# Optimization experiments

Hardware: AMD Instinct MI355X
Metric: run time of the kernel (lower is better)

Reference implementation:

```python
import jax, jax.numpy as jnp
import numpy as np

B, NH, NQ, NK, D = 2, 12, 2048, 2048, 64


def setup_inputs() -> dict:
    k0 = jax.random.key(0)
    k1, k2, k3, k4 = jax.random.split(k0, 4)
    return {
        "query": jax.random.normal(k1, (B, NH, NQ, D), dtype=jnp.float32),
        "key": jax.random.normal(k2, (B, NH, NK, D), dtype=jnp.float32),
        "value": jax.random.normal(k3, (B, NH, NK, D), dtype=jnp.float32),
        "mask": jnp.zeros((B, 1, NQ, NK), dtype=jnp.float32),
        "bias": jax.random.normal(k4, (NQ + NK + 1, NH), dtype=jnp.float32) * 0.02,
    }


def reference(query, key, value, mask, bias):
    head_size = query.shape[-1]
    nq = query.shape[-2]
    nk = key.shape[-2]
    # scores [B, H, Q, K]
    qk = jnp.einsum("bhqd,bhkd->bhqk", query, key) / jnp.sqrt(jnp.float32(head_size)).astype(query.dtype)
    # relative position bias: table [(nq+nk+1), nh] gathered at pos_q - pos_k + nk
    pos_qk = jnp.arange(nq)[:, None] - jnp.arange(nk)[None, :] + nk  # [Q, K]
    bias_qk = bias[pos_qk]                      # [Q, K, H]
    bias_qk = jnp.transpose(bias_qk, (2, 0, 1))[None]  # [1, H, Q, K]
    qk = qk + bias_qk + mask
    attn = jax.nn.softmax(qk, axis=-1)
    return jnp.einsum("bhqk,bhkd->bhqd", attn, value)
```

## Files before the change

### kernel.cpp

```cpp
#include <hip/hip_runtime.h>

#define NB  2
#define NH  12
#define NQ  2048
#define NKV 2048
#define DH  64
#define KVB 64
#define BH  (NB * NH)

#define L2E 1.44269504088896f
#define QSCL (0.125f * L2E)

typedef __attribute__((ext_vector_type(8))) short bf16x8;
typedef __attribute__((ext_vector_type(4))) short bf16x4;
typedef __attribute__((ext_vector_type(4))) float f32x4;
typedef __attribute__((ext_vector_type(2))) unsigned short u16x2;

#define EXP2F(x) __builtin_amdgcn_exp2f(x)

#define WS_KB   0u
#define WS_VT   6291456u
#define WS_NEED 12582912u

__device__ __forceinline__ unsigned short f2bf(float f) {
    unsigned int u = __float_as_uint(f);
    u += 0x7FFFu + ((u >> 16) & 1u);
    return (unsigned short)(u >> 16);
}
__device__ __forceinline__ float bf2f(unsigned short h) {
    return __uint_as_float((unsigned int)h << 16);
}
__device__ __forceinline__ int permk6(int k6) {
    return (k6 & 32) + ((k6 & 12) << 1) + ((k6 & 16) >> 2) + (k6 & 3);
}

__global__ __launch_bounds__(256)
void conv_kv(const float* __restrict__ K, const float* __restrict__ V,
             unsigned short* __restrict__ Kb, unsigned short* __restrict__ Vt)
{
    const int tid = threadIdx.x;
    const int kvt = blockIdx.x & 31;
    const int bh  = blockIdx.x >> 5;
    const int kv0 = kvt * 64;

    const float* ksrc = K + ((size_t)bh * NKV + kv0) * DH;
    const float* vsrc = V + ((size_t)bh * NKV + kv0) * DH;
    unsigned short* kdst = Kb + ((size_t)bh * NKV + kv0) * DH;
    unsigned short* vdst = Vt + (size_t)bh * DH * NKV + kv0;

    __shared__ float Ts[64][65];

#pragma unroll
    for (int p = 0; p < 2; ++p) {
        const int ch = p * 256 + tid;
        const int row = ch >> 3, c8 = (ch & 7) * 8;
        const float4 f0 = *(const float4*)(ksrc + (size_t)row * DH + c8);
        const float4 f1 = *(const float4*)(ksrc + (size_t)row * DH + c8 + 4);
        bf16x8 o;
        o[0] = (short)f2bf(f0.x); o[1] = (short)f2bf(f0.y);
        o[2] = (short)f2bf(f0.z); o[3] = (short)f2bf(f0.w);
        o[4] = (short)f2bf(f1.x); o[5] = (short)f2bf(f1.y);
        o[6] = (short)f2bf(f1.z); o[7] = (short)f2bf(f1.w);
        *(bf16x8*)(kdst + (size_t)row * DH + c8) = o;
    }
#pragma unroll
    for (int p = 0; p < 4; ++p) {
        const int fi = p * 1024 + tid * 4;
        const int row = fi >> 6, col = fi & 63;
        const float4 f = *(const float4*)(vsrc + (size_t)row * DH + col);
        Ts[row][col] = f.x; Ts[row][col + 1] = f.y;
        Ts[row][col + 2] = f.z; Ts[row][col + 3] = f.w;
    }
    __syncthreads();
#pragma unroll
    for (int p = 0; p < 2; ++p) {
        const int ch = p * 256 + tid;
        const int d = ch >> 3, c8 = (ch & 7) * 8;
        bf16x8 o;
#pragma unroll
        for (int j = 0; j < 8; ++j) o[j] = (short)f2bf(Ts[c8 + j][d]);
        unsigned short* vrow = vdst + (size_t)d * NKV;
        *(uint2*)(vrow + permk6(c8))     = ((const uint2*)&o)[0];
        *(uint2*)(vrow + permk6(c8 + 4)) = ((const uint2*)&o)[1];
    }
}

#define ARENA_BYTES 45312
#define KS_OFF 8448
#define VS_OFF 26880
#define BUF_STRIDE 9216

__global__ __launch_bounds__(512, 2)
void attn_fwd(const unsigned short* __restrict__ Kb, const unsigned short* __restrict__ Vt,
              const float* __restrict__ Q, const float* __restrict__ M,
              const float* __restrict__ Bias, float* __restrict__ O)
{
    const int tid  = threadIdx.x;
    const int w    = tid >> 6;
    const int wq   = w >> 1;
    const int wk   = w & 1;
    const int lane = tid & 63;
    const int l16  = lane & 15;
    const int g    = lane >> 4;

    const int qt = blockIdx.x & 31;
    const int bh = blockIdx.x >> 5;
    const int h  = bh % NH;
    const int b  = bh / NH;
    const int q0 = qt * 64;

    __shared__ __align__(16) char arena[ARENA_BYTES];
    unsigned short* bias2 = (unsigned short*)arena;

    for (int x = tid; x < 2112; x += 512) {
        const unsigned short v = f2bf(L2E * Bias[(size_t)(q0 + 1 + x) * NH + h]);
        bias2[2111 - x] = v;
        if (x <= 2110) bias2[2112 + 2110 - x] = v;
    }

    const float* qptr = Q + ((size_t)bh * NQ + q0 + wq * 16 + l16) * DH;
    bf16x8 qa[2];
#pragma unroll
    for (int dc = 0; dc < 2; ++dc) {
        const float4 f0 = *(const float4*)(qptr + dc * 32 + g * 8);
        const float4 f1 = *(const float4*)(qptr + dc * 32 + g * 8 + 4);
        qa[dc][0] = (short)f2bf(f0.x * QSCL); qa[dc][1] = (short)f2bf(f0.y * QSCL);
        qa[dc][2] = (short)f2bf(f0.z * QSCL); qa[dc][3] = (short)f2bf(f0.w * QSCL);
        qa[dc][4] = (short)f2bf(f1.x * QSCL); qa[dc][5] = (short)f2bf(f1.y * QSCL);
        qa[dc][6] = (short)f2bf(f1.z * QSCL); qa[dc][7] = (short)f2bf(f1.w * QSCL);
    }

    f32x4 o[4];
#pragma unroll
    for (int nt = 0; nt < 4; ++nt) { o[nt][0]=0.f; o[nt][1]=0.f; o[nt][2]=0.f; o[nt][3]=0.f; }
    float m_r = -1e30f;
    float l_r = 0.f;

    const unsigned short* kbB = Kb + (size_t)bh * NKV * DH;
    const unsigned short* vtB = Vt + (size_t)bh * DH * NKV;
    const float* mbase = M + (size_t)b * NQ * NKV
                           + (size_t)(q0 + wq * 16 + l16) * NKV + wk * 32 + g * 4;

    const int srow = tid >> 3, sc8 = (tid & 7) * 8;
    const int ldoff = srow * 144 + sc8 * 2;

    bf16x8 krB, vrB;
    float4 mr4[2], mrn4[2];
    krB = *(const bf16x8*)(kbB + (size_t)srow * DH + sc8);
    vrB = *(const bf16x8*)(vtB + (size_t)srow * NKV + sc8);
#pragma unroll
    for (int nt = 0; nt < 2; ++nt) mr4[nt] = *(const float4*)(mbase + nt * 16);

    *(bf16x8*)(arena + KS_OFF + ldoff) = krB;
    *(bf16x8*)(arena + VS_OFF + ldoff) = vrB;
    krB = *(const bf16x8*)(kbB + (size_t)(64 + srow) * DH + sc8);
    vrB = *(const bf16x8*)(vtB + (size_t)srow * NKV + 64 + sc8);
    __syncthreads();

    int cur = 0;
    for (int t = 0; t < NKV / KVB; ++t) {
        const int kv0 = t * KVB;
        const int tn  = ((t + 1) & (NKV / KVB - 1)) * KVB;
        const int t2  = ((t + 2) & (NKV / KVB - 1)) * KVB;
        const int nxt = cur ^ 1;

        *(bf16x8*)(arena + KS_OFF + nxt * BUF_STRIDE + ldoff) = krB;
        *(bf16x8*)(arena + VS_OFF + nxt * BUF_STRIDE + ldoff) = vrB;
        krB = *(const bf16x8*)(kbB + (size_t)(t2 + srow) * DH + sc8);
        vrB = *(const bf16x8*)(vtB + (size_t)srow * NKV + t2 + sc8);
#pragma unroll
        for (int nt = 0; nt < 2; ++nt) mrn4[nt] = *(const float4*)(mbase + tn + nt * 16);

        const unsigned short (*Ks)[72] = (const unsigned short(*)[72])(arena + KS_OFF + cur * BUF_STRIDE);
        const unsigned short (*Vs)[72] = (const unsigned short(*)[72])(arena + VS_OFF + cur * BUF_STRIDE);

        f32x4 s[2];
#pragma unroll
        for (int nt = 0; nt < 2; ++nt) {
            f32x4 acc; acc[0]=0.f; acc[1]=0.f; acc[2]=0.f; acc[3]=0.f;
            const int kvrow = wk * 32 + nt * 16 + l16;
            const bf16x8 kb0 = *(const bf16x8*)(&Ks[kvrow][g * 8]);
            const bf16x8 kb1 = *(const bf16x8*)(&Ks[kvrow][32 + g * 8]);
            acc = __builtin_amdgcn_mfma_f32_16x16x32_bf16(kb0, qa[0], acc, 0, 0, 0);
            acc = __builtin_amdgcn_mfma_f32_16x16x32_bf16(kb1, qa[1], acc, 0, 0, 0);
            s[nt] = acc;
        }

        bf16x8 va2[4];
#pragma unroll
        for (int nt = 0; nt < 4; ++nt)
            va2[nt] = *(const bf16x8*)(&Vs[nt * 16 + l16][wk * 32 + g * 8]);

        const int ib0 = (wq * 16 + l16) - (kv0 + wk * 32 + g * 4) + 2047;
#pragma unroll
        for (int nt = 0; nt < 2; ++nt) {
            const int j0 = 2111 - (ib0 - nt * 16);
            const int r  = j0 & 1;
            const unsigned short* bp = bias2 + r * 2112 + (j0 - r);
            const u16x2 b01 = *(const u16x2*)(bp);
            const u16x2 b23 = *(const u16x2*)(bp + 2);
            s[nt][0] += __fmaf_rn(nt ? mr4[1].x : mr4[0].x, L2E, bf2f(b01[0]));
            s[nt][1] += __fmaf_rn(nt ? mr4[1].y : mr4[0].y, L2E, bf2f(b01[1]));
            s[nt][2] += __fmaf_rn(nt ? mr4[1].z : mr4[0].z, L2E, bf2f(b23[0]));
            s[nt][3] += __fmaf_rn(nt ? mr4[1].w : mr4[0].w, L2E, bf2f(b23[1]));
        }

        const float x0  = fmaxf(fmaxf(s[0][0], s[0][1]), s[0][2]);
        const float x1  = fmaxf(fmaxf(s[0][3], s[1][0]), s[1][1]);
        const float x2  = fmaxf(s[1][2], s[1][3]);
        const float lmx = fmaxf(fmaxf(x0, x1), x2);
        if (__any(lmx > m_r + 8.0f)) {
            float mx = lmx;
            mx = fmaxf(mx, __shfl_xor(mx, 16));
            mx = fmaxf(mx, __shfl_xor(mx, 32));
            const float mn = fmaxf(m_r, mx);
            const float alpha = EXP2F(m_r - mn);
            m_r = mn;
            l_r *= alpha;
#pragma unroll
            for (int nt = 0; nt < 4; ++nt) {
                o[nt][0] *= alpha; o[nt][1] *= alpha;
                o[nt][2] *= alpha; o[nt][3] *= alpha;
            }
        }
        f32x4 pv[2];
#pragma unroll
        for (int nt = 0; nt < 2; ++nt) {
            pv[nt][0] = EXP2F(s[nt][0] - m_r);
            pv[nt][1] = EXP2F(s[nt][1] - m_r);
            pv[nt][2] = EXP2F(s[nt][2] - m_r);
            pv[nt][3] = EXP2F(s[nt][3] - m_r);
        }
        l_r += ((pv[0][0] + pv[0][1]) + (pv[0][2] + pv[0][3]))
             + ((pv[1][0] + pv[1][1]) + (pv[1][2] + pv[1][3]));

        mr4[0] = mrn4[0]; mr4[1] = mrn4[1];

        union { unsigned u[4]; bf16x8 v; } pb8;
        asm("v_cvt_pk_bf16_f32 %0, %1, %2" : "=v"(pb8.u[0]) : "v"(pv[0][0]), "v"(pv[0][1]));
        asm("v_cvt_pk_bf16_f32 %0, %1, %2" : "=v"(pb8.u[1]) : "v"(pv[0][2]), "v"(pv[0][3]));
        asm("v_cvt_pk_bf16_f32 %0, %1, %2" : "=v"(pb8.u[2]) : "v"(pv[1][0]), "v"(pv[1][1]));
        asm("v_cvt_pk_bf16_f32 %0, %1, %2" : "=v"(pb8.u[3]) : "v"(pv[1][2]), "v"(pv[1][3]));

#pragma unroll
        for (int nt = 0; nt < 4; ++nt)
            o[nt] = __builtin_amdgcn_mfma_f32_16x16x32_bf16(va2[nt], pb8.v, o[nt], 0, 0, 0);

        __syncthreads();
        cur = nxt;
    }

    l_r += __shfl_xor(l_r, 16);
    l_r += __shfl_xor(l_r, 32);

    float (*mO)[64][17] = (float(*)[64][17])(arena + KS_OFF);
    float* mML          = (float*)(arena + KS_OFF + 17408);

    __syncthreads();
    if (wk == 1) {
#pragma unroll
        for (int nt = 0; nt < 4; ++nt) {
#pragma unroll
            for (int reg = 0; reg < 4; ++reg)
                mO[wq][nt * 16 + g * 4 + reg][l16] = o[nt][reg];
        }
        if (g == 0) {
            mML[wq * 16 + l16]      = m_r;
            mML[64 + wq * 16 + l16] = l_r;
        }
    }
    __syncthreads();
    if (wk == 0) {
        const float m1 = mML[wq * 16 + l16];
        const float l1 = mML[64 + wq * 16 + l16];
        const float mn = fmaxf(m_r, m1);
        const float a0 = EXP2F(m_r - mn);
        const float a1 = EXP2F(m1 - mn);
        const float inv = 1.f / (l_r * a0 + l1 * a1);
        float* obase = O + ((size_t)bh * NQ + q0 + wq * 16 + l16) * DH;
#pragma unroll
        for (int nt = 0; nt < 4; ++nt) {
            float4 ov;
            ov.x = (o[nt][0] * a0 + mO[wq][nt * 16 + g * 4 + 0][l16] * a1) * inv;
            ov.y = (o[nt][1] * a0 + mO[wq][nt * 16 + g * 4 + 1][l16] * a1) * inv;
            ov.z = (o[nt][2] * a0 + mO[wq][nt * 16 + g * 4 + 2][l16] * a1) * inv;
            ov.w = (o[nt][3] * a0 + mO[wq][nt * 16 + g * 4 + 3][l16] * a1) * inv;
            *(float4*)(obase + nt * 16 + g * 4) = ov;
        }
    }
}

__global__ __launch_bounds__(256, 3)
void attn_full(const float* __restrict__ Q, const float* __restrict__ K,
               const float* __restrict__ V, const float* __restrict__ M,
               const float* __restrict__ Bias, float* __restrict__ O)
{
    const int tid  = threadIdx.x;
    const int wv   = tid >> 6;
    const int lane = tid & 63;
    const int l16  = lane & 15;
    const int g    = lane >> 4;

    const int qt = blockIdx.x & 31;
    const int h  = (blockIdx.x >> 5) % NH;
    const int b  = blockIdx.x / (32 * NH);
    const int q0 = qt * 64;

    __shared__ float bias_s[2112];
    __shared__ unsigned short Ks[64][72];
    __shared__ unsigned short Vs[64][72];
    __shared__ unsigned short Ps[4][16][72];

    for (int i = tid; i < 2112; i += 256)
        bias_s[i] = Bias[(size_t)(q0 + 1 + i) * NH + h];

    const float* qptr = Q + (((size_t)b * NH + h) * NQ + q0 + wv * 16 + l16) * DH;
    bf16x8 qa[2];
#pragma unroll
    for (int dc = 0; dc < 2; ++dc) {
        const float4 f0 = *(const float4*)(qptr + dc * 32 + g * 8);
        const float4 f1 = *(const float4*)(qptr + dc * 32 + g * 8 + 4);
        qa[dc][0] = (short)f2bf(f0.x); qa[dc][1] = (short)f2bf(f0.y);
        qa[dc][2] = (short)f2bf(f0.z); qa[dc][3] = (short)f2bf(f0.w);
        qa[dc][4] = (short)f2bf(f1.x); qa[dc][5] = (short)f2bf(f1.y);
        qa[dc][6] = (short)f2bf(f1.z); qa[dc][7] = (short)f2bf(f1.w);
    }

    f32x4 o[4];
#pragma unroll
    for (int nt = 0; nt < 4; ++nt) { o[nt][0]=0.f; o[nt][1]=0.f; o[nt][2]=0.f; o[nt][3]=0.f; }
    float m_r[4] = {-1e30f, -1e30f, -1e30f, -1e30f};
    float l_r[4] = {0.f, 0.f, 0.f, 0.f};

    const float* kbase = K + ((size_t)b * NH + h) * NKV * DH;
    const float* vbase = V + ((size_t)b * NH + h) * NKV * DH;
    const float* mrow[4];
#pragma unroll
    for (int r = 0; r < 4; ++r)
        mrow[r] = M + (size_t)b * NQ * NKV + (size_t)(q0 + wv * 16 + g * 4 + r) * NKV + l16;

    const int r0 = tid >> 4, c0 = (tid & 15) * 4;

    float4 kr[4], vr[4];
    float  mr[4][4];
#pragma unroll
    for (int i = 0; i < 4; ++i) {
        kr[i] = *(const float4*)(kbase + (size_t)(i * 16 + r0) * DH + c0);
        vr[i] = *(const float4*)(vbase + (size_t)(i * 16 + r0) * DH + c0);
    }
#pragma unroll
    for (int r = 0; r < 4; ++r)
#pragma unroll
        for (int nt = 0; nt < 4; ++nt) mr[r][nt] = mrow[r][nt * 16];

    for (int t = 0; t < NKV / 64; ++t) {
        const int kv0 = t * 64;
        const int kvn = ((t + 1) & 31) * 64;

        __syncthreads();
#pragma unroll
        for (int i = 0; i < 4; ++i) {
            unsigned short* dst = &Ks[i * 16 + r0][c0];
            dst[0] = f2bf(kr[i].x); dst[1] = f2bf(kr[i].y);
            dst[2] = f2bf(kr[i].z); dst[3] = f2bf(kr[i].w);
        }
#pragma unroll
        for (int i = 0; i < 4; ++i) {
            const int rr = i * 16 + r0;
            Vs[c0 + 0][rr] = f2bf(vr[i].x); Vs[c0 + 1][rr] = f2bf(vr[i].y);
            Vs[c0 + 2][rr] = f2bf(vr[i].z); Vs[c0 + 3][rr] = f2bf(vr[i].w);
        }
#pragma unroll
        for (int i = 0; i < 4; ++i) {
            kr[i] = *(const float4*)(kbase + (size_t)(kvn + i * 16 + r0) * DH + c0);
            vr[i] = *(const float4*)(vbase + (size_t)(kvn + i * 16 + r0) * DH + c0);
        }
        __syncthreads();

        f32x4 s[4];
#pragma unroll
        for (int nt = 0; nt < 4; ++nt) {
            f32x4 acc; acc[0]=0.f; acc[1]=0.f; acc[2]=0.f; acc[3]=0.f;
            const bf16x8 kb0 = *(const bf16x8*)(&Ks[nt * 16 + l16][g * 8]);
            const bf16x8 kb1 = *(const bf16x8*)(&Ks[nt * 16 + l16][32 + g * 8]);
            acc = __builtin_amdgcn_mfma_f32_16x16x32_bf16(qa[0], kb0, acc, 0, 0, 0);
            acc = __builtin_amdgcn_mfma_f32_16x16x32_bf16(qa[1], kb1, acc, 0, 0, 0);
            s[nt] = acc;
        }

#pragma unroll
        for (int r = 0; r < 4; ++r) {
            const int qr = wv * 16 + g * 4 + r;
#pragma unroll
            for (int nt = 0; nt < 4; ++nt) {
                float x = s[nt][r] * 0.125f + mr[r][nt];
                x += bias_s[qr - (kv0 + nt * 16 + l16) + 2047];
                s[nt][r] = x;
            }
            float mx = fmaxf(fmaxf(s[0][r], s[1][r]), fmaxf(s[2][r], s[3][r]));
            mx = fmaxf(mx, __shfl_xor(mx, 1));
            mx = fmaxf(mx, __shfl_xor(mx, 2));
            mx = fmaxf(mx, __shfl_xor(mx, 4));
            mx = fmaxf(mx, __shfl_xor(mx, 8));
            const float mo = m_r[r];
            const float mn = fmaxf(mo, mx);
            m_r[r] = mn;
            const float alpha = __expf(mo - mn);
            float p[4], rs = 0.f;
#pragma unroll
            for (int nt = 0; nt < 4; ++nt) { p[nt] = __expf(s[nt][r] - mn); rs += p[nt]; }
            rs += __shfl_xor(rs, 1);
            rs += __shfl_xor(rs, 2);
            rs += __shfl_xor(rs, 4);
            rs += __shfl_xor(rs, 8);
            l_r[r] = l_r[r] * alpha + rs;
#pragma unroll
            for (int nt = 0; nt < 4; ++nt) o[nt][r] *= alpha;
#pragma unroll
            for (int nt = 0; nt < 4; ++nt)
                Ps[wv][g * 4 + r][nt * 16 + l16] = f2bf(p[nt]);
        }

#pragma unroll
        for (int r = 0; r < 4; ++r)
#pragma unroll
            for (int nt = 0; nt < 4; ++nt) mr[r][nt] = mrow[r][kvn + nt * 16];

#pragma unroll
        for (int kc = 0; kc < 2; ++kc) {
            const bf16x8 pa = *(const bf16x8*)(&Ps[wv][l16][kc * 32 + g * 8]);
#pragma unroll
            for (int nt = 0; nt < 4; ++nt) {
                const bf16x8 vb = *(const bf16x8*)(&Vs[nt * 16 + l16][kc * 32 + g * 8]);
                o[nt] = __builtin_amdgcn_mfma_f32_16x16x32_bf16(pa, vb, o[nt], 0, 0, 0);
            }
        }
    }

    float* obase = O + (((size_t)b * NH + h) * NQ + q0 + wv * 16) * DH;
#pragma unroll
    for (int r = 0; r < 4; ++r) {
        const float inv = 1.f / l_r[r];
#pragma unroll
        for (int nt = 0; nt < 4; ++nt)
            obase[(size_t)(g * 4 + r) * DH + nt * 16 + l16] = o[nt][r] * inv;
    }
}

extern "C" void kernel_launch(void* const* d_in, const int* in_sizes, int n_in,
                              void* d_out, int out_size, void* d_ws, size_t ws_size,
                              hipStream_t stream) {
    const float* Q    = (const float*)d_in[0];
    const float* K    = (const float*)d_in[1];
    const float* V    = (const float*)d_in[2];
    const float* M    = (const float*)d_in[3];
    const float* Bias = (const float*)d_in[4];
    float* O = (float*)d_out;

    if (ws_size >= (size_t)WS_NEED) {
        unsigned short* Kb = (unsigned short*)((char*)d_ws + WS_KB);
        unsigned short* Vt = (unsigned short*)((char*)d_ws + WS_VT);
        conv_kv<<<dim3(BH * 32), dim3(256), 0, stream>>>(K, V, Kb, Vt);
        attn_fwd<<<dim3(BH * 32), dim3(512), 0, stream>>>(Kb, Vt, Q, M, Bias, O);
    } else {
        attn_full<<<dim3(BH * 32), dim3(256), 0, stream>>>(Q, K, V, M, Bias, O);
    }
}
```

Measured before the change: 78.31 us.

## Halve block to 256 threads with each wave handling two query sub-tiles

Each workgroup shrinks from 8 to 4 waves, and every wave now processes two 16-row query sub-tiles against the same K/V fragments it reads from LDS. This reuses each LDS read of K and V across two MFMA chains and halves the per-block LDS read traffic per query row. In exchange, register pressure per wave goes up (two sets of accumulators, scores and masks), each thread stages two rows of K/V per tile, and there are fewer waves per block to hide latency.

```diff
diff --git a/kernel.cpp b/kernel.cpp
--- a/kernel.cpp
+++ b/kernel.cpp
@@ -90,14 +90,14 @@
 #define VS_OFF 26880
 #define BUF_STRIDE 9216
 
-__global__ __launch_bounds__(512, 2)
+__global__ __launch_bounds__(256, 2)
 void attn_fwd(const unsigned short* __restrict__ Kb, const unsigned short* __restrict__ Vt,
               const float* __restrict__ Q, const float* __restrict__ M,
               const float* __restrict__ Bias, float* __restrict__ O)
 {
     const int tid  = threadIdx.x;
     const int w    = tid >> 6;
-    const int wq   = w >> 1;
+    const int qp   = w >> 1;
     const int wk   = w & 1;
     const int lane = tid & 63;
     const int l16  = lane & 15;
@@ -112,49 +112,64 @@
     __shared__ __align__(16) char arena[ARENA_BYTES];
     unsigned short* bias2 = (unsigned short*)arena;
 
-    for (int x = tid; x < 2112; x += 512) {
+    for (int x = tid; x < 2112; x += 256) {
         const unsigned short v = f2bf(L2E * Bias[(size_t)(q0 + 1 + x) * NH + h]);
         bias2[2111 - x] = v;
         if (x <= 2110) bias2[2112 + 2110 - x] = v;
     }
 
-    const float* qptr = Q + ((size_t)bh * NQ + q0 + wq * 16 + l16) * DH;
-    bf16x8 qa[2];
-#pragma unroll
-    for (int dc = 0; dc < 2; ++dc) {
-        const float4 f0 = *(const float4*)(qptr + dc * 32 + g * 8);
-        const float4 f1 = *(const float4*)(qptr + dc * 32 + g * 8 + 4);
-        qa[dc][0] = (short)f2bf(f0.x * QSCL); qa[dc][1] = (short)f2bf(f0.y * QSCL);
-        qa[dc][2] = (short)f2bf(f0.z * QSCL); qa[dc][3] = (short)f2bf(f0.w * QSCL);
-        qa[dc][4] = (short)f2bf(f1.x * QSCL); qa[dc][5] = (short)f2bf(f1.y * QSCL);
-        qa[dc][6] = (short)f2bf(f1.z * QSCL); qa[dc][7] = (short)f2bf(f1.w * QSCL);
-    }
-
-    f32x4 o[4];
-#pragma unroll
-    for (int nt = 0; nt < 4; ++nt) { o[nt][0]=0.f; o[nt][1]=0.f; o[nt][2]=0.f; o[nt][3]=0.f; }
-    float m_r = -1e30f;
-    float l_r = 0.f;
+    bf16x8 qa[2][2];
+#pragma unroll
+    for (int sub = 0; sub < 2; ++sub) {
+        const float* qptr = Q + ((size_t)bh * NQ + q0 + qp * 32 + sub * 16 + l16) * DH;
+#pragma unroll
+        for (int dc = 0; dc < 2; ++dc) {
+            const float4 f0 = *(const float4*)(qptr + dc * 32 + g * 8);
+            const float4 f1 = *(const float4*)(qptr + dc * 32 + g * 8 + 4);
+            qa[sub][dc][0] = (short)f2bf(f0.x * QSCL); qa[sub][dc][1] = (short)f2bf(f0.y * QSCL);
+            qa[sub][dc][2] = (short)f2bf(f0.z * QSCL); qa[sub][dc][3] = (short)f2bf(f0.w * QSCL);
+            qa[sub][dc][4] = (short)f2bf(f1.x * QSCL); qa[sub][dc][5] = (short)f2bf(f1.y * QSCL);
+            qa[sub][dc][6] = (short)f2bf(f1.z * QSCL); qa[sub][dc][7] = (short)f2bf(f1.w * QSCL);
+        }
+    }
+
+    f32x4 o0[4], o1[4];
+#pragma unroll
+    for (int nt = 0; nt < 4; ++nt) {
+        o0[nt][0]=0.f; o0[nt][1]=0.f; o0[nt][2]=0.f; o0[nt][3]=0.f;
+        o1[nt][0]=0.f; o1[nt][1]=0.f; o1[nt][2]=0.f; o1[nt][3]=0.f;
+    }
+    float m_r[2] = {-1e30f, -1e30f};
+    float l_r[2] = {0.f, 0.f};
 
     const unsigned short* kbB = Kb + (size_t)bh * NKV * DH;
     const unsigned short* vtB = Vt + (size_t)bh * DH * NKV;
-    const float* mbase = M + (size_t)b * NQ * NKV
-                           + (size_t)(q0 + wq * 16 + l16) * NKV + wk * 32 + g * 4;
+    const float* mb0 = M + (size_t)b * NQ * NKV
+                         + (size_t)(q0 + qp * 32 + l16) * NKV + wk * 32 + g * 4;
+    const float* mb1 = mb0 + 16 * NKV;
 
     const int srow = tid >> 3, sc8 = (tid & 7) * 8;
-    const int ldoff = srow * 144 + sc8 * 2;
-
-    bf16x8 krB, vrB;
-    float4 mr4[2], mrn4[2];
-    krB = *(const bf16x8*)(kbB + (size_t)srow * DH + sc8);
-    vrB = *(const bf16x8*)(vtB + (size_t)srow * NKV + sc8);
-#pragma unroll
-    for (int nt = 0; nt < 2; ++nt) mr4[nt] = *(const float4*)(mbase + nt * 16);
-
-    *(bf16x8*)(arena + KS_OFF + ldoff) = krB;
-    *(bf16x8*)(arena + VS_OFF + ldoff) = vrB;
-    krB = *(const bf16x8*)(kbB + (size_t)(64 + srow) * DH + sc8);
-    vrB = *(const bf16x8*)(vtB + (size_t)srow * NKV + 64 + sc8);
+
+    bf16x8 krB[2], vrB[2];
+    float4 mr4[2][2], mrn4[2][2];
+#pragma unroll
+    for (int p = 0; p < 2; ++p) {
+        krB[p] = *(const bf16x8*)(kbB + (size_t)(p * 32 + srow) * DH + sc8);
+        vrB[p] = *(const bf16x8*)(vtB + (size_t)(p * 32 + srow) * NKV + sc8);
+    }
+#pragma unroll
+    for (int nt = 0; nt < 2; ++nt) {
+        mr4[0][nt] = *(const float4*)(mb0 + nt * 16);
+        mr4[1][nt] = *(const float4*)(mb1 + nt * 16);
+    }
+#pragma unroll
+    for (int p = 0; p < 2; ++p) {
+        const int ldoff = (p * 32 + srow) * 144 + sc8 * 2;
+        *(bf16x8*)(arena + KS_OFF + ldoff) = krB[p];
+        *(bf16x8*)(arena + VS_OFF + ldoff) = vrB[p];
+        krB[p] = *(const bf16x8*)(kbB + (size_t)(64 + p * 32 + srow) * DH + sc8);
+        vrB[p] = *(const bf16x8*)(vtB + (size_t)(p * 32 + srow) * NKV + 64 + sc8);
+    }
     __syncthreads();
 
     int cur = 0;
@@ -164,94 +179,132 @@
         const int t2  = ((t + 2) & (NKV / KVB - 1)) * KVB;
         const int nxt = cur ^ 1;
 
-        *(bf16x8*)(arena + KS_OFF + nxt * BUF_STRIDE + ldoff) = krB;
-        *(bf16x8*)(arena + VS_OFF + nxt * BUF_STRIDE + ldoff) = vrB;
-        krB = *(const bf16x8*)(kbB + (size_t)(t2 + srow) * DH + sc8);
-        vrB = *(const bf16x8*)(vtB + (size_t)srow * NKV + t2 + sc8);
-#pragma unroll
-        for (int nt = 0; nt < 2; ++nt) mrn4[nt] = *(const float4*)(mbase + tn + nt * 16);
+#pragma unroll
+        for (int p = 0; p < 2; ++p) {
+            const int ldoff = (p * 32 + srow) * 144 + sc8 * 2;
+            *(bf16x8*)(arena + KS_OFF + nxt * BUF_STRIDE + ldoff) = krB[p];
+            *(bf16x8*)(arena + VS_OFF + nxt * BUF_STRIDE + ldoff) = vrB[p];
+            krB[p] = *(const bf16x8*)(kbB + (size_t)(t2 + p * 32 + srow) * DH + sc8);
+            vrB[p] = *(const bf16x8*)(vtB + (size_t)(p * 32 + srow) * NKV + t2 + sc8);
+        }
+#pragma unroll
+        for (int nt = 0; nt < 2; ++nt) {
+            mrn4[0][nt] = *(const float4*)(mb0 + tn + nt * 16);
+            mrn4[1][nt] = *(const float4*)(mb1 + tn + nt * 16);
+        }
 
         const unsigned short (*Ks)[72] = (const unsigned short(*)[72])(arena + KS_OFF + cur * BUF_STRIDE);
         const unsigned short (*Vs)[72] = (const unsigned short(*)[72])(arena + VS_OFF + cur * BUF_STRIDE);
 
-        f32x4 s[2];
+        bf16x8 kb0[2], kb1[2];
 #pragma unroll
         for (int nt = 0; nt < 2; ++nt) {
-            f32x4 acc; acc[0]=0.f; acc[1]=0.f; acc[2]=0.f; acc[3]=0.f;
             const int kvrow = wk * 32 + nt * 16 + l16;
-            const bf16x8 kb0 = *(const bf16x8*)(&Ks[kvrow][g * 8]);
-            const bf16x8 kb1 = *(const bf16x8*)(&Ks[kvrow][32 + g * 8]);
-            acc = __builtin_amdgcn_mfma_f32_16x16x32_bf16(kb0, qa[0], acc, 0, 0, 0);
-            acc = __builtin_amdgcn_mfma_f32_16x16x32_bf16(kb1, qa[1], acc, 0, 0, 0);
-            s[nt] = acc;
-        }
-
+            kb0[nt] = *(const bf16x8*)(&Ks[kvrow][g * 8]);
+            kb1[nt] = *(const bf16x8*)(&Ks[kvrow][32 + g * 8]);
+        }
         bf16x8 va2[4];
 #pragma unroll
         for (int nt = 0; nt < 4; ++nt)
             va2[nt] = *(const bf16x8*)(&Vs[nt * 16 + l16][wk * 32 + g * 8]);
 
-        const int ib0 = (wq * 16 + l16) - (kv0 + wk * 32 + g * 4) + 2047;
+        f32x4 s0[2], s1[2];
 #pragma unroll
         for (int nt = 0; nt < 2; ++nt) {
-            const int j0 = 2111 - (ib0 - nt * 16);
-            const int r  = j0 & 1;
-            const unsigned short* bp = bias2 + r * 2112 + (j0 - r);
-            const u16x2 b01 = *(const u16x2*)(bp);
-            const u16x2 b23 = *(const u16x2*)(bp + 2);
-            s[nt][0] += __fmaf_rn(nt ? mr4[1].x : mr4[0].x, L2E, bf2f(b01[0]));
-            s[nt][1] += __fmaf_rn(nt ? mr4[1].y : mr4[0].y, L2E, bf2f(b01[1]));
-            s[nt][2] += __fmaf_rn(nt ? mr4[1].z : mr4[0].z, L2E, bf2f(b23[0]));
-            s[nt][3] += __fmaf_rn(nt ? mr4[1].w : mr4[0].w, L2E, bf2f(b23[1]));
-        }
-
-        const float x0  = fmaxf(fmaxf(s[0][0], s[0][1]), s[0][2]);
-        const float x1  = fmaxf(fmaxf(s[0][3], s[1][0]), s[1][1]);
-        const float x2  = fmaxf(s[1][2], s[1][3]);
-        const float lmx = fmaxf(fmaxf(x0, x1), x2);
-        if (__any(lmx > m_r + 8.0f)) {
-            float mx = lmx;
-            mx = fmaxf(mx, __shfl_xor(mx, 16));
-            mx = fmaxf(mx, __shfl_xor(mx, 32));
-            const float mn = fmaxf(m_r, mx);
-            const float alpha = EXP2F(m_r - mn);
-            m_r = mn;
-            l_r *= alpha;
-#pragma unroll
-            for (int nt = 0; nt < 4; ++nt) {
-                o[nt][0] *= alpha; o[nt][1] *= alpha;
-                o[nt][2] *= alpha; o[nt][3] *= alpha;
-            }
-        }
-        f32x4 pv[2];
+            f32x4 a0; a0[0]=0.f; a0[1]=0.f; a0[2]=0.f; a0[3]=0.f;
+            f32x4 a1 = a0;
+            a0 = __builtin_amdgcn_mfma_f32_16x16x32_bf16(kb0[nt], qa[0][0], a0, 0, 0, 0);
+            a0 = __builtin_amdgcn_mfma_f32_16x16x32_bf16(kb1[nt], qa[0][1], a0, 0, 0, 0);
+            a1 = __builtin_amdgcn_mfma_f32_16x16x32_bf16(kb0[nt], qa[1][0], a1, 0, 0, 0);
+            a1 = __builtin_amdgcn_mfma_f32_16x16x32_bf16(kb1[nt], qa[1][1], a1, 0, 0, 0);
+            s0[nt] = a0; s1[nt] = a1;
+        }
+
+        const int qbase = qp * 32 + l16 - (kv0 + wk * 32 + g * 4) + 2047;
+#pragma unroll
+        for (int sub = 0; sub < 2; ++sub) {
+            f32x4* s = sub ? s1 : s0;
+#pragma unroll
+            for (int nt = 0; nt < 2; ++nt) {
+                const int j0 = 2111 - (qbase + sub * 16 - nt * 16);
+                const int r  = j0 & 1;
+                const unsigned short* bp = bias2 + r * 2112 + (j0 - r);
+                const u16x2 b01 = *(const u16x2*)(bp);
+                const u16x2 b23 = *(const u16x2*)(bp + 2);
+                const float4 mm = mr4[sub][nt];
+                s[nt][0] += __fmaf_rn(mm.x, L2E, bf2f(b01[0]));
+                s[nt][1] += __fmaf_rn(mm.y, L2E, bf2f(b01[1]));
+                s[nt][2] += __fmaf_rn(mm.z, L2E, bf2f(b23[0]));
+                s[nt][3] += __fmaf_rn(mm.w, L2E, bf2f(b23[1]));
+            }
+        }
+
+        f32x4 pv0[2], pv1[2];
+#pragma unroll
+        for (int sub = 0; sub < 2; ++sub) {
+            f32x4* s  = sub ? s1 : s0;
+            f32x4* pv = sub ? pv1 : pv0;
+            f32x4* oo = sub ? o1 : o0;
+            const float x0  = fmaxf(fmaxf(s[0][0], s[0][1]), s[0][2]);
+            const float x1  = fmaxf(fmaxf(s[0][3], s[1][0]), s[1][1]);
+            const float x2  = fmaxf(s[1][2], s[1][3]);
+            const float lmx = fmaxf(fmaxf(x0, x1), x2);
+            if (__any(lmx > m_r[sub] + 8.0f)) {
+                float mx = lmx;
+                mx = fmaxf(mx, __shfl_xor(mx, 16));
+                mx = fmaxf(mx, __shfl_xor(mx, 32));
+                const float mn = fmaxf(m_r[sub], mx);
+                const float alpha = EXP2F(m_r[sub] - mn);
+                m_r[sub] = mn;
+                l_r[sub] *= alpha;
+#pragma unroll
+                for (int nt = 0; nt < 4; ++nt) {
+                    oo[nt][0] *= alpha; oo[nt][1] *= alpha;
+                    oo[nt][2] *= alpha; oo[nt][3] *= alpha;
+                }
+            }
+#pragma unroll
+            for (int nt = 0; nt < 2; ++nt) {
+                pv[nt][0] = EXP2F(s[nt][0] - m_r[sub]);
+                pv[nt][1] = EXP2F(s[nt][1] - m_r[sub]);
+                pv[nt][2] = EXP2F(s[nt][2] - m_r[sub]);
+                pv[nt][3] = EXP2F(s[nt][3] - m_r[sub]);
+            }
+            l_r[sub] += ((pv[0][0] + pv[0][1]) + (pv[0][2] + pv[0][3]))
+                      + ((pv[1][0] + pv[1][1]) + (pv[1][2] + pv[1][3]));
+        }
+
 #pragma unroll
         for (int nt = 0; nt < 2; ++nt) {
-            pv[nt][0] = EXP2F(s[nt][0] - m_r);
-            pv[nt][1] = EXP2F(s[nt][1] - m_r);
-            pv[nt][2] = EXP2F(s[nt][2] - m_r);
-            pv[nt][3] = EXP2F(s[nt][3] - m_r);
-        }
-        l_r += ((pv[0][0] + pv[0][1]) + (pv[0][2] + pv[0][3]))
-             + ((pv[1][0] + pv[1][1]) + (pv[1][2] + pv[1][3]));
-
-        mr4[0] = mrn4[0]; mr4[1] = mrn4[1];
-
-        union { unsigned u[4]; bf16x8 v; } pb8;
-        asm("v_cvt_pk_bf16_f32 %0, %1, %2" : "=v"(pb8.u[0]) : "v"(pv[0][0]), "v"(pv[0][1]));
-        asm("v_cvt_pk_bf16_f32 %0, %1, %2" : "=v"(pb8.u[1]) : "v"(pv[0][2]), "v"(pv[0][3]));
-        asm("v_cvt_pk_bf16_f32 %0, %1, %2" : "=v"(pb8.u[2]) : "v"(pv[1][0]), "v"(pv[1][1]));
-        asm("v_cvt_pk_bf16_f32 %0, %1, %2" : "=v"(pb8.u[3]) : "v"(pv[1][2]), "v"(pv[1][3]));
-
-#pragma unroll
-        for (int nt = 0; nt < 4; ++nt)
-            o[nt] = __builtin_amdgcn_mfma_f32_16x16x32_bf16(va2[nt], pb8.v, o[nt], 0, 0, 0);
+            mr4[0][nt] = mrn4[0][nt];
+            mr4[1][nt] = mrn4[1][nt];
+        }
+
+        union { unsigned u[4]; bf16x8 v; } pb0, pb1;
+        asm("v_cvt_pk_bf16_f32 %0, %1, %2" : "=v"(pb0.u[0]) : "v"(pv0[0][0]), "v"(pv0[0][1]));
+        asm("v_cvt_pk_bf16_f32 %0, %1, %2" : "=v"(pb0.u[1]) : "v"(pv0[0][2]), "v"(pv0[0][3]));
+        asm("v_cvt_pk_bf16_f32 %0, %1, %2" : "=v"(pb0.u[2]) : "v"(pv0[1][0]), "v"(pv0[1][1]));
+        asm("v_cvt_pk_bf16_f32 %0, %1, %2" : "=v"(pb0.u[3]) : "v"(pv0[1][2]), "v"(pv0[1][3]));
+        asm("v_cvt_pk_bf16_f32 %0, %1, %2" : "=v"(pb1.u[0]) : "v"(pv1[0][0]), "v"(pv1[0][1]));
+        asm("v_cvt_pk_bf16_f32 %0, %1, %2" : "=v"(pb1.u[1]) : "v"(pv1[0][2]), "v"(pv1[0][3]));
+        asm("v_cvt_pk_bf16_f32 %0, %1, %2" : "=v"(pb1.u[2]) : "v"(pv1[1][0]), "v"(pv1[1][1]));
+        asm("v_cvt_pk_bf16_f32 %0, %1, %2" : "=v"(pb1.u[3]) : "v"(pv1[1][2]), "v"(pv1[1][3]));
+
+#pragma unroll
+        for (int nt = 0; nt < 4; ++nt) {
+            o0[nt] = __builtin_amdgcn_mfma_f32_16x16x32_bf16(va2[nt], pb0.v, o0[nt], 0, 0, 0);
+            o1[nt] = __builtin_amdgcn_mfma_f32_16x16x32_bf16(va2[nt], pb1.v, o1[nt], 0, 0, 0);
+        }
 
         __syncthreads();
         cur = nxt;
     }
 
-    l_r += __shfl_xor(l_r, 16);
-    l_r += __shfl_xor(l_r, 32);
+#pragma unroll
+    for (int sub = 0; sub < 2; ++sub) {
+        l_r[sub] += __shfl_xor(l_r[sub], 16);
+        l_r[sub] += __shfl_xor(l_r[sub], 32);
+    }
 
     float (*mO)[64][17] = (float(*)[64][17])(arena + KS_OFF);
     float* mML          = (float*)(arena + KS_OFF + 17408);
@@ -259,33 +312,42 @@
     __syncthreads();
     if (wk == 1) {
 #pragma unroll
-        for (int nt = 0; nt < 4; ++nt) {
-#pragma unroll
-            for (int reg = 0; reg < 4; ++reg)
-                mO[wq][nt * 16 + g * 4 + reg][l16] = o[nt][reg];
-        }
-        if (g == 0) {
-            mML[wq * 16 + l16]      = m_r;
-            mML[64 + wq * 16 + l16] = l_r;
+        for (int sub = 0; sub < 2; ++sub) {
+            const f32x4* oo = sub ? o1 : o0;
+            const int st = qp * 2 + sub;
+#pragma unroll
+            for (int nt = 0; nt < 4; ++nt)
+#pragma unroll
+                for (int reg = 0; reg < 4; ++reg)
+                    mO[st][nt * 16 + g * 4 + reg][l16] = oo[nt][reg];
+            if (g == 0) {
+                mML[st * 16 + l16]      = m_r[sub];
+                mML[64 + st * 16 + l16] = l_r[sub];
+            }
         }
     }
     __syncthreads();
     if (wk == 0) {
-        const float m1 = mML[wq * 16 + l16];
-        const float l1 = mML[64 + wq * 16 + l16];
-        const float mn = fmaxf(m_r, m1);
-        const float a0 = EXP2F(m_r - mn);
-        const float a1 = EXP2F(m1 - mn);
-        const float inv = 1.f / (l_r * a0 + l1 * a1);
-        float* obase = O + ((size_t)bh * NQ + q0 + wq * 16 + l16) * DH;
-#pragma unroll
-        for (int nt = 0; nt < 4; ++nt) {
-            float4 ov;
-            ov.x = (o[nt][0] * a0 + mO[wq][nt * 16 + g * 4 + 0][l16] * a1) * inv;
-            ov.y = (o[nt][1] * a0 + mO[wq][nt * 16 + g * 4 + 1][l16] * a1) * inv;
-            ov.z = (o[nt][2] * a0 + mO[wq][nt * 16 + g * 4 + 2][l16] * a1) * inv;
-            ov.w = (o[nt][3] * a0 + mO[wq][nt * 16 + g * 4 + 3][l16] * a1) * inv;
-            *(float4*)(obase + nt * 16 + g * 4) = ov;
+#pragma unroll
+        for (int sub = 0; sub < 2; ++sub) {
+            const f32x4* oo = sub ? o1 : o0;
+            const int st = qp * 2 + sub;
+            const float m1 = mML[st * 16 + l16];
+            const float l1 = mML[64 + st * 16 + l16];
+            const float mn = fmaxf(m_r[sub], m1);
+            const float a0 = EXP2F(m_r[sub] - mn);
+            const float a1 = EXP2F(m1 - mn);
+            const float inv = 1.f / (l_r[sub] * a0 + l1 * a1);
+            float* obase = O + ((size_t)bh * NQ + q0 + qp * 32 + sub * 16 + l16) * DH;
+#pragma unroll
+            for (int nt = 0; nt < 4; ++nt) {
+                float4 ov;
+                ov.x = (oo[nt][0] * a0 + mO[st][nt * 16 + g * 4 + 0][l16] * a1) * inv;
+                ov.y = (oo[nt][1] * a0 + mO[st][nt * 16 + g * 4 + 1][l16] * a1) * inv;
+                ov.z = (oo[nt][2] * a0 + mO[st][nt * 16 + g * 4 + 2][l16] * a1) * inv;
+                ov.w = (oo[nt][3] * a0 + mO[st][nt * 16 + g * 4 + 3][l16] * a1) * inv;
+                *(float4*)(obase + nt * 16 + g * 4) = ov;
+            }
         }
     }
 }
@@ -461,7 +523,7 @@
         unsigned short* Kb = (unsigned short*)((char*)d_ws + WS_KB);
         unsigned short* Vt = (unsigned short*)((char*)d_ws + WS_VT);
         conv_kv<<<dim3(BH * 32), dim3(256), 0, stream>>>(K, V, Kb, Vt);
-        attn_fwd<<<dim3(BH * 32), dim3(512), 0, stream>>>(Kb, Vt, Q, M, Bias, O);
+        attn_fwd<<<dim3(BH * 32), dim3(256), 0, stream>>>(Kb, Vt, Q, M, Bias, O);
     } else {
         attn_full<<<dim3(BH * 32), dim3(256), 0, stream>>>(Q, K, V, M, Bias, O);
     }
```

Result: slower. 88.51 us (+13.0%).
